# Kernel tuning notes

Hardware: AMD Instinct MI355X
Metric: run time of the kernel (lower is better)

Reference implementation:

```python
import jax, jax.numpy as jnp
import numpy as np
from math import sqrt

B, D, N, L, H, P = 32, 64, 254, 16, 128, 96  # batch, channels, patch_num, patch_len, hidden, pred_len


def positional_encoding(n, d):
    # standard sinusoidal PE, shape (n, d)
    pos = np.arange(n)[:, None].astype(np.float32)
    div = np.exp(np.arange(0, d, 2).astype(np.float32) * (-np.log(10000.0) / d))
    pe = np.zeros((n, d), dtype=np.float32)
    pe[:, 0::2] = np.sin(pos * div)
    pe[:, 1::2] = np.cos(pos * div)
    return jnp.asarray(pe)


def setup_inputs() -> dict:
    key = jax.random.key(0)
    ks = jax.random.split(key, 7)
    s = 0.05
    return {
        "x": jax.random.normal(ks[0], (B, D, N, L), dtype=jnp.float32),
        "W_enc": jax.random.normal(ks[1], (L, H), dtype=jnp.float32) * s,
        "b_enc": jax.random.normal(ks[2], (H,), dtype=jnp.float32) * s,
        "W1": jax.random.normal(ks[3], (L, H), dtype=jnp.float32) * s,
        "b1": jax.random.normal(ks[4], (H,), dtype=jnp.float32) * s,
        "W2": jax.random.normal(ks[5], (H, P), dtype=jnp.float32) * s,
        "b2": jax.random.normal(ks[6], (P,), dtype=jnp.float32) * s,
        "pos_embed": positional_encoding(N, H),  # buffer, not learned
    }


def reference(x, W_enc, b_enc, W1, b1, W2, b2, pos_embed):
    p = x  # detached clone in torch; same values
    # encode patches: (B,D,N,L) @ (L,H) -> (B,D,N,H), plus PE (N,H) broadcast
    c = jnp.einsum("bdnl,lh->bdnh", x, W_enc) + b_enc + pos_embed
    # score_i = sum_j c_i . c_j / sqrt(H)  ==  c_i . (sum_j c_j) / sqrt(H)
    csum = jnp.sum(c, axis=-2, keepdims=True)            # (B,D,1,H)
    score = jnp.sum(c * csum, axis=-1, keepdims=True) / sqrt(H)  # (B,D,N,1)
    weight = score / jnp.sum(jnp.abs(score), axis=-2, keepdims=True)
    pooled = jnp.sum(x * weight, axis=-2)                # (B,D,L)
    # FeedForward (dropout inactive at eval)
    h = jax.nn.leaky_relu(pooled @ W1 + b1, negative_slope=0.2)
    out = h @ W2 + b2                                    # (B,D,P)
    return out.transpose(0, 2, 1), p                     # (B,P,D), (B,D,N,L)
```

## Files before the change

### kernel.cpp

```cpp
#include <hip/hip_runtime.h>
#include <hip/hip_bf16.h>

#define B_ 32
#define D_ 64
#define N_ 254
#define L_ 16
#define H_ 128
#define P_ 96
#define PAIRS (B_*D_)
#define XPAIR (N_*L_)
#define OUT0  (B_*P_*D_)

#define WS_M    128
#define WS_VK   384
#define WS_BW   400
#define WS_BK   416
#define WS_G    432
#define WS_PK   4496
#define WS_KP   4752

__global__ __launch_bounds__(256) void preK(const float* __restrict__ pos,
                                            float* __restrict__ ws) {
    __shared__ float red[256];
    int t = threadIdx.x;
    int h = t & 127, j = t >> 7;
    int n0 = blockIdx.x * 16;
    float acc = 0.f;
    #pragma unroll
    for (int r = 0; r < 8; r++) {
        int n = n0 + j + 2 * r;
        if (n < N_) acc += pos[n * H_ + h];
    }
    red[t] = acc;
    __syncthreads();
    if (t < 128) ws[WS_KP + blockIdx.x * 128 + t] = red[t] + red[t + 128];
}

__global__ __launch_bounds__(128) void pre2b(const float* __restrict__ W_enc,
                                             const float* __restrict__ b_enc,
                                             const float* __restrict__ pos,
                                             float* __restrict__ ws) {
    __shared__ float Ks[128], bL[128], pLDS[128], red[128], red2[128];
    __shared__ float WL[2048];
    int t = threadIdx.x;
    int n = blockIdx.x;

    {
        float b = b_enc[t];
        float s = 254.f * b;
        #pragma unroll
        for (int g = 0; g < 16; g++) s += ws[WS_KP + g * 128 + t];
        Ks[t] = s;
        bL[t] = b;
    }

    if (n < N_) {
        pLDS[t] = pos[n * H_ + t];
        __syncthreads();
        {
            int l = t >> 3, c = t & 7;
            const float* w = W_enc + l * H_ + c * 16;
            const float* p = pLDS + c * 16;
            float s = 0.f;
            #pragma unroll
            for (int i = 0; i < 16; i++) s += p[i] * w[i];
            red[t] = s;
            red2[t] = pLDS[t] * Ks[t];
        }
        __syncthreads();
        if (t < 16) {
            float s = 0.f;
            #pragma unroll
            for (int c = 0; c < 8; c++) s += red[t * 8 + c];
            ws[WS_G + n * 16 + t] = s;
        }
        if (t >= 64) {
            int lane = t - 64;
            float s = red2[lane] + red2[lane + 64];
            for (int off = 32; off; off >>= 1) s += __shfl_down(s, off);
            if (lane == 0) ws[WS_PK + n] = s;
        }
    } else {
        for (int i = t; i < 512; i += 128) {
            float4 v = ((const float4*)W_enc)[i];
            float* p = &WL[i * 4];
            p[0] = v.x; p[1] = v.y; p[2] = v.z; p[3] = v.w;
        }
        __syncthreads();
        #pragma unroll
        for (int e0 = 0; e0 < 2; e0++) {
            int e = e0 * 128 + t;
            int l1 = e >> 4, l2 = e & 15;
            float s = 0.f;
            for (int h = 0; h < H_; h++) s += WL[l1 * H_ + h] * WL[l2 * H_ + h];
            ws[WS_M + e] = s;
        }
        if (t < 16) {
            float s1 = 0.f, s2 = 0.f;
            for (int h = 0; h < H_; h++) {
                float w = WL[t * H_ + h];
                s1 += w * Ks[h];
                s2 += w * bL[h];
            }
            ws[WS_VK + t] = s1;
            ws[WS_BW + t] = s2;
        }
        if (t == 16) {
            float s = 0.f;
            for (int h = 0; h < H_; h++) s += bL[h] * Ks[h];
            ws[WS_BK] = s;
        }
    }
}

__global__ __launch_bounds__(256) void mainker(const float* __restrict__ x,
                                               const float* __restrict__ W1,
                                               const float* __restrict__ b1,
                                               const float* __restrict__ W2,
                                               const float* __restrict__ b2,
                                               const float* __restrict__ ws,
                                               float* __restrict__ out) {
    __shared__ float xf[N_ * 17 + 16];
    __shared__ float red[256];
    __shared__ float scoreS[N_];
    __shared__ float xsS[16], vS[16], pooledS[16], hS[128];
    __shared__ float s0S, denomS;

    int t  = threadIdx.x;
    int bd = blockIdx.x;

    const float4* xv = (const float4*)(x + (size_t)bd * XPAIR);
    float4*       cv = (float4*)(out + OUT0) + (size_t)bd * (XPAIR / 4);
    for (int i = t; i < XPAIR / 4; i += 256) {
        float4 v = xv[i];
        cv[i] = v;
        int idx = i * 4;
        int n = idx >> 4, l = idx & 15;
        float* p = &xf[n * 17 + l];
        p[0] = v.x; p[1] = v.y; p[2] = v.z; p[3] = v.w;
    }
    __syncthreads();

    {
        int l = t & 15, g = t >> 4;
        float s = 0.f;
        for (int n = g; n < N_; n += 16) s += xf[n * 17 + l];
        red[t] = s;
    }
    __syncthreads();
    if (t < 16) {
        float s = 0.f;
        for (int g = 0; g < 16; g++) s += red[g * 16 + t];
        xsS[t] = s;
    }
    __syncthreads();

    if (t < 16) {
        float s = ws[WS_VK + t];
        for (int l2 = 0; l2 < 16; l2++) s += xsS[l2] * ws[WS_M + l2 * 16 + t];
        vS[t] = s;
    } else if (t == 16) {
        float s = ws[WS_BK];
        for (int l = 0; l < 16; l++) s += xsS[l] * ws[WS_BW + l];
        s0S = s;
    }
    __syncthreads();

    if (t < N_) {
        const float* Gn = ws + WS_G + t * 16;
        float s = s0S + ws[WS_PK + t];
        #pragma unroll
        for (int l = 0; l < 16; l++) s += xf[t * 17 + l] * vS[l] + xsS[l] * Gn[l];
        scoreS[t] = s;
    }
    __syncthreads();

    if (t < 64) {
        float s = 0.f;
        for (int n = t; n < N_; n += 64) s += fabsf(scoreS[n]);
        for (int off = 32; off; off >>= 1) s += __shfl_down(s, off);
        if (t == 0) denomS = s;
    }
    __syncthreads();
    float inv = 1.0f / denomS;

    {
        int l = t & 15, g = t >> 4;
        float s = 0.f;
        for (int n = g; n < N_; n += 16) s += xf[n * 17 + l] * scoreS[n];
        red[t] = s;
    }
    __syncthreads();
    if (t < 16) {
        float s = 0.f;
        for (int g = 0; g < 16; g++) s += red[g * 16 + t];
        pooledS[t] = s * inv;
    }
    __syncthreads();

    if (t < 128) {
        float s = b1[t];
        #pragma unroll
        for (int l = 0; l < 16; l++) s += pooledS[l] * W1[l * H_ + t];
        hS[t] = s > 0.f ? s : 0.2f * s;
    }
    __syncthreads();

    if (t < 96) {
        float s = b2[t];
        for (int j = 0; j < 128; j++) s += hS[j] * W2[j * P_ + t];
        int b = bd >> 6, d = bd & 63;
        out[b * (P_ * D_) + t * D_ + d] = s;
    }
}

extern "C" void kernel_launch(void* const* d_in, const int* in_sizes, int n_in,
                              void* d_out, int out_size, void* d_ws, size_t ws_size,
                              hipStream_t stream) {
    const float* x     = (const float*)d_in[0];
    const float* W_enc = (const float*)d_in[1];
    const float* b_enc = (const float*)d_in[2];
    const float* W1    = (const float*)d_in[3];
    const float* b1    = (const float*)d_in[4];
    const float* W2    = (const float*)d_in[5];
    const float* b2    = (const float*)d_in[6];
    const float* pos   = (const float*)d_in[7];
    float* ws  = (float*)d_ws;
    float* out = (float*)d_out;

    hipLaunchKernelGGL(preK,   dim3(16),    dim3(256), 0, stream, pos, ws);
    hipLaunchKernelGGL(pre2b,  dim3(255),   dim3(128), 0, stream, W_enc, b_enc, pos, ws);
    hipLaunchKernelGGL(mainker, dim3(PAIRS), dim3(256), 0, stream, x, W1, b1, W2, b2, ws, out);
}
```

Baseline: 119.3 us.

## Map one wavefront per (b,d) pair with register-resident patches and shuffle reductions

The main kernel now gives each 64-lane wavefront one (b,d) pair, with four pairs per block, instead of one pair per 256-thread block. Each lane holds up to four patch rows in registers. Column sums, scores, the abs-sum denominator and the pooled vector are computed with cross-lane shuffles in place of LDS staging and block barriers. Workspace tables (M, G, pK) are staged once per block in shared memory and shared by the four waves. This removes many __syncthreads and the LDS copy of x, at the cost of higher register pressure and per-wave serial FFN loops.

```diff
diff --git a/kernel.cpp b/kernel.cpp
--- a/kernel.cpp
+++ b/kernel.cpp
@@ -120,97 +120,147 @@
                                                const float* __restrict__ b2,
                                                const float* __restrict__ ws,
                                                float* __restrict__ out) {
-    __shared__ float xf[N_ * 17 + 16];
-    __shared__ float red[256];
-    __shared__ float scoreS[N_];
-    __shared__ float xsS[16], vS[16], pooledS[16], hS[128];
-    __shared__ float s0S, denomS;
-
-    int t  = threadIdx.x;
-    int bd = blockIdx.x;
-
-    const float4* xv = (const float4*)(x + (size_t)bd * XPAIR);
-    float4*       cv = (float4*)(out + OUT0) + (size_t)bd * (XPAIR / 4);
-    for (int i = t; i < XPAIR / 4; i += 256) {
-        float4 v = xv[i];
-        cv[i] = v;
-        int idx = i * 4;
-        int n = idx >> 4, l = idx & 15;
-        float* p = &xf[n * 17 + l];
-        p[0] = v.x; p[1] = v.y; p[2] = v.z; p[3] = v.w;
+    __shared__ float Wsm[304];
+    __shared__ float Gp[N_ * 20];
+    __shared__ float pKs[N_];
+    __shared__ float vSh[4][16];
+    __shared__ float hSh[4][128];
+
+    int t = threadIdx.x;
+    int wv = t >> 6, lane = t & 63;
+    int bd = blockIdx.x * 4 + wv;
+
+    const float* xp = x + (size_t)bd * XPAIR;
+    float*       cp = out + OUT0 + (size_t)bd * XPAIR;
+
+    float4 xr[4][4];
+    #pragma unroll
+    for (int r = 0; r < 4; r++) {
+        int n = lane + 64 * r;
+        if (n < N_) {
+            const float4* row = (const float4*)(xp + n * 16);
+            #pragma unroll
+            for (int j = 0; j < 4; j++) xr[r][j] = row[j];
+        } else {
+            #pragma unroll
+            for (int j = 0; j < 4; j++) xr[r][j] = make_float4(0.f, 0.f, 0.f, 0.f);
+        }
+    }
+    #pragma unroll
+    for (int r = 0; r < 4; r++) {
+        int n = lane + 64 * r;
+        if (n < N_) {
+            float4* row = (float4*)(cp + n * 16);
+            #pragma unroll
+            for (int j = 0; j < 4; j++) row[j] = xr[r][j];
+        }
+    }
+
+    for (int i = t; i < 304; i += 256) Wsm[i] = ws[WS_M + i];
+    for (int i = t; i < N_;  i += 256) pKs[i] = ws[WS_PK + i];
+    for (int i = t; i < 1016; i += 256) {
+        float4 g = ((const float4*)(ws + WS_G))[i];
+        int idx = i * 4, n = idx >> 4, l = idx & 15;
+        *(float4*)&Gp[n * 20 + l] = g;
     }
     __syncthreads();
 
+    float xs[16];
+    #pragma unroll
+    for (int k = 0; k < 4; k++) {
+        float4 a = xr[0][k], b = xr[1][k], c = xr[2][k], d = xr[3][k];
+        xs[4*k+0] = a.x + b.x + c.x + d.x;
+        xs[4*k+1] = a.y + b.y + c.y + d.y;
+        xs[4*k+2] = a.z + b.z + c.z + d.z;
+        xs[4*k+3] = a.w + b.w + c.w + d.w;
+    }
+    #pragma unroll
+    for (int off = 32; off; off >>= 1) {
+        #pragma unroll
+        for (int l = 0; l < 16; l++) xs[l] += __shfl_xor(xs[l], off);
+    }
+
+    if (lane < 16) {
+        float acc = Wsm[256 + lane];
+        #pragma unroll
+        for (int l2 = 0; l2 < 16; l2++) acc += xs[l2] * Wsm[l2 * 16 + lane];
+        vSh[wv][lane] = acc;
+    }
+    __builtin_amdgcn_wave_barrier();
+    float v[16];
+    #pragma unroll
+    for (int k = 0; k < 4; k++) *(float4*)&v[4*k] = *(const float4*)&vSh[wv][4*k];
+
+    float s0 = Wsm[288];
+    #pragma unroll
+    for (int l = 0; l < 16; l++) s0 += xs[l] * Wsm[272 + l];
+
+    float sc[4];
+    #pragma unroll
+    for (int r = 0; r < 4; r++) {
+        int n = lane + 64 * r;
+        if (n < N_) {
+            float acc = s0 + pKs[n];
+            const float* g = &Gp[n * 20];
+            #pragma unroll
+            for (int k = 0; k < 4; k++) {
+                float4 gv = *(const float4*)&g[4*k];
+                float4 xv = xr[r][k];
+                acc += xv.x * v[4*k+0] + xv.y * v[4*k+1] + xv.z * v[4*k+2] + xv.w * v[4*k+3];
+                acc += gv.x * xs[4*k+0] + gv.y * xs[4*k+1] + gv.z * xs[4*k+2] + gv.w * xs[4*k+3];
+            }
+            sc[r] = acc;
+        } else sc[r] = 0.f;
+    }
+
+    float den = fabsf(sc[0]) + fabsf(sc[1]) + fabsf(sc[2]) + fabsf(sc[3]);
+    #pragma unroll
+    for (int off = 32; off; off >>= 1) den += __shfl_xor(den, off);
+    float inv = 1.0f / den;
+
+    float pl[16];
+    #pragma unroll
+    for (int k = 0; k < 4; k++) {
+        float4 a = xr[0][k], b = xr[1][k], c = xr[2][k], d = xr[3][k];
+        pl[4*k+0] = a.x*sc[0] + b.x*sc[1] + c.x*sc[2] + d.x*sc[3];
+        pl[4*k+1] = a.y*sc[0] + b.y*sc[1] + c.y*sc[2] + d.y*sc[3];
+        pl[4*k+2] = a.z*sc[0] + b.z*sc[1] + c.z*sc[2] + d.z*sc[3];
+        pl[4*k+3] = a.w*sc[0] + b.w*sc[1] + c.w*sc[2] + d.w*sc[3];
+    }
+    #pragma unroll
+    for (int off = 32; off; off >>= 1) {
+        #pragma unroll
+        for (int l = 0; l < 16; l++) pl[l] += __shfl_xor(pl[l], off);
+    }
+    #pragma unroll
+    for (int l = 0; l < 16; l++) pl[l] *= inv;
+
     {
-        int l = t & 15, g = t >> 4;
-        float s = 0.f;
-        for (int n = g; n < N_; n += 16) s += xf[n * 17 + l];
-        red[t] = s;
-    }
-    __syncthreads();
-    if (t < 16) {
-        float s = 0.f;
-        for (int g = 0; g < 16; g++) s += red[g * 16 + t];
-        xsS[t] = s;
-    }
-    __syncthreads();
-
-    if (t < 16) {
-        float s = ws[WS_VK + t];
-        for (int l2 = 0; l2 < 16; l2++) s += xsS[l2] * ws[WS_M + l2 * 16 + t];
-        vS[t] = s;
-    } else if (t == 16) {
-        float s = ws[WS_BK];
-        for (int l = 0; l < 16; l++) s += xsS[l] * ws[WS_BW + l];
-        s0S = s;
-    }
-    __syncthreads();
-
-    if (t < N_) {
-        const float* Gn = ws + WS_G + t * 16;
-        float s = s0S + ws[WS_PK + t];
-        #pragma unroll
-        for (int l = 0; l < 16; l++) s += xf[t * 17 + l] * vS[l] + xsS[l] * Gn[l];
-        scoreS[t] = s;
-    }
-    __syncthreads();
-
-    if (t < 64) {
-        float s = 0.f;
-        for (int n = t; n < N_; n += 64) s += fabsf(scoreS[n]);
-        for (int off = 32; off; off >>= 1) s += __shfl_down(s, off);
-        if (t == 0) denomS = s;
-    }
-    __syncthreads();
-    float inv = 1.0f / denomS;
+        float a0 = b1[lane], a1 = b1[lane + 64];
+        #pragma unroll
+        for (int l = 0; l < 16; l++) {
+            a0 += pl[l] * W1[l * H_ + lane];
+            a1 += pl[l] * W1[l * H_ + lane + 64];
+        }
+        hSh[wv][lane]      = a0 > 0.f ? a0 : 0.2f * a0;
+        hSh[wv][lane + 64] = a1 > 0.f ? a1 : 0.2f * a1;
+    }
+    __builtin_amdgcn_wave_barrier();
 
     {
-        int l = t & 15, g = t >> 4;
-        float s = 0.f;
-        for (int n = g; n < N_; n += 16) s += xf[n * 17 + l] * scoreS[n];
-        red[t] = s;
-    }
-    __syncthreads();
-    if (t < 16) {
-        float s = 0.f;
-        for (int g = 0; g < 16; g++) s += red[g * 16 + t];
-        pooledS[t] = s * inv;
-    }
-    __syncthreads();
-
-    if (t < 128) {
-        float s = b1[t];
-        #pragma unroll
-        for (int l = 0; l < 16; l++) s += pooledS[l] * W1[l * H_ + t];
-        hS[t] = s > 0.f ? s : 0.2f * s;
-    }
-    __syncthreads();
-
-    if (t < 96) {
-        float s = b2[t];
-        for (int j = 0; j < 128; j++) s += hS[j] * W2[j * P_ + t];
         int b = bd >> 6, d = bd & 63;
-        out[b * (P_ * D_) + t * D_ + d] = s;
+        float* outp = out + b * (P_ * D_) + d;
+        float acc0 = b2[lane];
+        float acc1 = (lane < 32) ? b2[lane + 64] : 0.f;
+        const float* hw = &hSh[wv][0];
+        #pragma unroll 8
+        for (int j = 0; j < 128; j++) {
+            float hj = hw[j];
+            acc0 += hj * W2[j * P_ + lane];
+            if (lane < 32) acc1 += hj * W2[j * P_ + lane + 64];
+        }
+        outp[lane * D_] = acc0;
+        if (lane < 32) outp[(lane + 64) * D_] = acc1;
     }
 }
 
@@ -228,7 +278,7 @@
     float* ws  = (float*)d_ws;
     float* out = (float*)d_out;
 
-    hipLaunchKernelGGL(preK,   dim3(16),    dim3(256), 0, stream, pos, ws);
-    hipLaunchKernelGGL(pre2b,  dim3(255),   dim3(128), 0, stream, W_enc, b_enc, pos, ws);
-    hipLaunchKernelGGL(mainker, dim3(PAIRS), dim3(256), 0, stream, x, W1, b1, W2, b2, ws, out);
-}
+    hipLaunchKernelGGL(preK,    dim3(16),  dim3(256), 0, stream, pos, ws);
+    hipLaunchKernelGGL(pre2b,   dim3(255), dim3(128), 0, stream, W_enc, b_enc, pos, ws);
+    hipLaunchKernelGGL(mainker, dim3(512), dim3(256), 0, stream, x, W1, b1, W2, b2, ws, out);
+}
```

Measured after the change: 151.7 us. +27.2%, slower.

## Split FFN into separate batched kernel and use nontemporal stores for x copy

Applied to the files above, without the earlier changes.

Moves the per-pair feed-forward (W1 then W2 matvecs) out of the main per-(b,d) kernel into a new kernel. That kernel processes 64 channels per block, so W1/W2 loads are reused across channels instead of being re-read by every pair block. The main kernel now writes the pooled vectors to workspace, uses nontemporal stores for the passthrough copy of x, and unrolls the score dot products with vector loads of G. This adds a fourth launch and a workspace round trip, and the new FFN kernel runs only 96 blocks.

```diff
diff --git a/kernel.cpp b/kernel.cpp
--- a/kernel.cpp
+++ b/kernel.cpp
@@ -11,6 +11,8 @@
 #define XPAIR (N_*L_)
 #define OUT0  (B_*P_*D_)
 
+typedef float float4n __attribute__((ext_vector_type(4)));
+
 #define WS_M    128
 #define WS_VK   384
 #define WS_BW   400
@@ -18,6 +20,7 @@
 #define WS_G    432
 #define WS_PK   4496
 #define WS_KP   4752
+#define WS_PL   8192
 
 __global__ __launch_bounds__(256) void preK(const float* __restrict__ pos,
                                             float* __restrict__ ws) {
@@ -113,29 +116,24 @@
     }
 }
 
-__global__ __launch_bounds__(256) void mainker(const float* __restrict__ x,
-                                               const float* __restrict__ W1,
-                                               const float* __restrict__ b1,
-                                               const float* __restrict__ W2,
-                                               const float* __restrict__ b2,
-                                               const float* __restrict__ ws,
-                                               float* __restrict__ out) {
-    __shared__ float xf[N_ * 17 + 16];
+__global__ __launch_bounds__(256) void mainker2(const float* __restrict__ x,
+                                                float* __restrict__ ws,
+                                                float* __restrict__ out) {
+    __shared__ float xf[N_ * 17];
     __shared__ float red[256];
     __shared__ float scoreS[N_];
-    __shared__ float xsS[16], vS[16], pooledS[16], hS[128];
+    __shared__ float xsS[16], vS[16];
     __shared__ float s0S, denomS;
 
     int t  = threadIdx.x;
     int bd = blockIdx.x;
 
-    const float4* xv = (const float4*)(x + (size_t)bd * XPAIR);
-    float4*       cv = (float4*)(out + OUT0) + (size_t)bd * (XPAIR / 4);
+    const float4n* xv = (const float4n*)(x + (size_t)bd * XPAIR);
+    float4n*       cv = (float4n*)(out + OUT0) + (size_t)bd * (XPAIR / 4);
     for (int i = t; i < XPAIR / 4; i += 256) {
-        float4 v = xv[i];
-        cv[i] = v;
-        int idx = i * 4;
-        int n = idx >> 4, l = idx & 15;
+        float4n v = xv[i];
+        __builtin_nontemporal_store(v, cv + i);
+        int idx = i * 4, n = idx >> 4, l = idx & 15;
         float* p = &xf[n * 17 + l];
         p[0] = v.x; p[1] = v.y; p[2] = v.z; p[3] = v.w;
     }
@@ -167,10 +165,18 @@
     __syncthreads();
 
     if (t < N_) {
-        const float* Gn = ws + WS_G + t * 16;
+        const float4* Gn = (const float4*)(ws + WS_G + t * 16);
+        float4 g0 = Gn[0], g1 = Gn[1], g2 = Gn[2], g3 = Gn[3];
+        const float* xr = &xf[t * 17];
         float s = s0S + ws[WS_PK + t];
-        #pragma unroll
-        for (int l = 0; l < 16; l++) s += xf[t * 17 + l] * vS[l] + xsS[l] * Gn[l];
+        s += xr[0]*vS[0] + xr[1]*vS[1] + xr[2]*vS[2] + xr[3]*vS[3]
+           + xr[4]*vS[4] + xr[5]*vS[5] + xr[6]*vS[6] + xr[7]*vS[7]
+           + xr[8]*vS[8] + xr[9]*vS[9] + xr[10]*vS[10] + xr[11]*vS[11]
+           + xr[12]*vS[12] + xr[13]*vS[13] + xr[14]*vS[14] + xr[15]*vS[15];
+        s += g0.x*xsS[0] + g0.y*xsS[1] + g0.z*xsS[2] + g0.w*xsS[3]
+           + g1.x*xsS[4] + g1.y*xsS[5] + g1.z*xsS[6] + g1.w*xsS[7]
+           + g2.x*xsS[8] + g2.y*xsS[9] + g2.z*xsS[10] + g2.w*xsS[11]
+           + g3.x*xsS[12] + g3.y*xsS[13] + g3.z*xsS[14] + g3.w*xsS[15];
         scoreS[t] = s;
     }
     __syncthreads();
@@ -182,7 +188,6 @@
         if (t == 0) denomS = s;
     }
     __syncthreads();
-    float inv = 1.0f / denomS;
 
     {
         int l = t & 15, g = t >> 4;
@@ -194,23 +199,61 @@
     if (t < 16) {
         float s = 0.f;
         for (int g = 0; g < 16; g++) s += red[g * 16 + t];
-        pooledS[t] = s * inv;
-    }
-    __syncthreads();
-
-    if (t < 128) {
-        float s = b1[t];
-        #pragma unroll
-        for (int l = 0; l < 16; l++) s += pooledS[l] * W1[l * H_ + t];
-        hS[t] = s > 0.f ? s : 0.2f * s;
-    }
-    __syncthreads();
-
-    if (t < 96) {
-        float s = b2[t];
-        for (int j = 0; j < 128; j++) s += hS[j] * W2[j * P_ + t];
-        int b = bd >> 6, d = bd & 63;
-        out[b * (P_ * D_) + t * D_ + d] = s;
+        ws[WS_PL + bd * 16 + t] = s / denomS;
+    }
+}
+
+__global__ __launch_bounds__(256) void ffnker(const float* __restrict__ W1,
+                                              const float* __restrict__ b1,
+                                              const float* __restrict__ W2,
+                                              const float* __restrict__ b2,
+                                              const float* __restrict__ ws,
+                                              float* __restrict__ out) {
+    __shared__ float pl[64 * 16];
+    __shared__ float hS[64 * 129];
+    int t  = threadIdx.x;
+    int b  = blockIdx.x / 3;
+    int pc = blockIdx.x % 3;
+
+    {
+        const float* src = ws + WS_PL + b * 1024;
+        for (int i = t; i < 1024; i += 256) pl[i] = src[i];
+    }
+    __syncthreads();
+
+    {
+        int j = t & 127, dg = t >> 7;
+        float w1r[16];
+        #pragma unroll
+        for (int l = 0; l < 16; l++) w1r[l] = W1[l * H_ + j];
+        float bj = b1[j];
+        for (int dd = 0; dd < 32; dd++) {
+            int d = dg * 32 + dd;
+            const float* pd = &pl[d * 16];
+            float a = bj;
+            #pragma unroll
+            for (int l = 0; l < 16; l++) a += pd[l] * w1r[l];
+            hS[d * 129 + j] = a > 0.f ? a : 0.2f * a;
+        }
+    }
+    __syncthreads();
+
+    {
+        int d  = t & 63, pg = t >> 6;
+        int p0 = pc * 32 + pg * 8;
+        float acc[8];
+        #pragma unroll
+        for (int k = 0; k < 8; k++) acc[k] = b2[p0 + k];
+        const float* hd = &hS[d * 129];
+        for (int j = 0; j < 128; j++) {
+            float hj = hd[j];
+            const float* w2 = W2 + j * P_ + p0;
+            #pragma unroll
+            for (int k = 0; k < 8; k++) acc[k] += hj * w2[k];
+        }
+        float* op = out + b * (P_ * D_) + d;
+        #pragma unroll
+        for (int k = 0; k < 8; k++) op[(p0 + k) * D_] = acc[k];
     }
 }
 
@@ -228,7 +271,8 @@
     float* ws  = (float*)d_ws;
     float* out = (float*)d_out;
 
-    hipLaunchKernelGGL(preK,   dim3(16),    dim3(256), 0, stream, pos, ws);
-    hipLaunchKernelGGL(pre2b,  dim3(255),   dim3(128), 0, stream, W_enc, b_enc, pos, ws);
-    hipLaunchKernelGGL(mainker, dim3(PAIRS), dim3(256), 0, stream, x, W1, b1, W2, b2, ws, out);
-}
+    hipLaunchKernelGGL(preK,     dim3(16),    dim3(256), 0, stream, pos, ws);
+    hipLaunchKernelGGL(pre2b,    dim3(255),   dim3(128), 0, stream, W_enc, b_enc, pos, ws);
+    hipLaunchKernelGGL(mainker2, dim3(PAIRS), dim3(256), 0, stream, x, ws, out);
+    hipLaunchKernelGGL(ffnker,   dim3(96),    dim3(256), 0, stream, W1, b1, W2, b2, ws, out);
+}
```

After: 132.4 us. 1.11x slower.
